# Optimization experiments

Measured on AMD Instinct MI355X. Metric: run time of the kernel, lower is better.

## Reference

```python
import jax, jax.numpy as jnp
import numpy as np

MARGIN = 1.0  # init kwarg
BIG = 1e9     # finite sentinel for masked reductions (dist in [0, 2])


def setup_inputs() -> dict:
    key = jax.random.key(0)
    k1, k2 = jax.random.split(key)
    embeddings = jax.random.normal(k1, (8192, 256), dtype=jnp.float32)
    labels = jax.random.randint(k2, (8192,), 0, 128)
    return {"embeddings": embeddings, "labels": labels}


def reference(embeddings, labels):
    # cosine distance matrix: 1 - x_hat @ x_hat^T, clamped at 0
    norm = jnp.linalg.norm(embeddings, axis=1, keepdims=True)
    x = embeddings / jnp.maximum(norm, 1e-12)  # matches F.normalize eps
    dist = jnp.clip(1.0 - x @ x.T, 0.0, None)  # (B, B)

    same = labels[:, None] == labels[None, :]
    eye = jnp.eye(labels.shape[0], dtype=bool)
    pos_mask = same & ~eye   # same label, different index
    neg_mask = ~same         # different label

    # hard mining: hardest positive (max dist), hardest negative (min dist)
    pos_dist = jnp.max(jnp.where(pos_mask, dist, -BIG), axis=1)  # (B,)
    neg_dist = jnp.min(jnp.where(neg_mask, dist, BIG), axis=1)   # (B,)

    valid = pos_mask.any(axis=1) & neg_mask.any(axis=1)          # (B,)
    per_anchor = jnp.maximum(pos_dist - neg_dist + MARGIN, 0.0)
    loss_sum = jnp.sum(jnp.where(valid, per_anchor, 0.0))
    count = jnp.sum(valid).astype(dist.dtype)
    return jnp.where(count > 0, loss_sum / jnp.maximum(count, 1.0), 0.0)
```

## Files before the change

kernel.cpp:

```cpp
#include <hip/hip_runtime.h>
#include <hip/hip_bf16.h>


constexpr int NB = 8192;
constexpr int ND = 256;
constexpr int BI = 256;
constexpr int BJ = 64;
constexpr int JSPLIT = 16;
constexpr int JRANGE = NB / JSPLIT;
constexpr int NITER = JRANGE / BJ;
constexpr int NCHUNK = ND / 8;

typedef __attribute__((ext_vector_type(8))) short bf16x8;
typedef __attribute__((ext_vector_type(4))) float f32x4;

typedef __attribute__((address_space(3))) unsigned int lds_u32;
typedef __attribute__((address_space(1))) const unsigned int g_u32;

__device__ inline void load_lds16(const unsigned short* g, unsigned short* l) {
    __builtin_amdgcn_global_load_lds((g_u32*)g, (lds_u32*)l, 16, 0, 0);
}

__device__ inline unsigned short f2bf(float v) {
    __hip_bfloat16 b = __float2bfloat16(v);
    return *reinterpret_cast<unsigned short*>(&b);
}

__global__ __launch_bounds__(256) void norm_kernel(const float* __restrict__ X,
                                                   unsigned short* __restrict__ Xbt,
                                                   float* accum, int* done) {
    __shared__ float tile[32][260];
    __shared__ float psum[32][8];
    __shared__ float rscale[32];
    const int t = threadIdx.x;
    const int rb = blockIdx.x * 32;
    if (blockIdx.x == 0 && t == 0) { accum[0] = 0.f; accum[1] = 0.f; *done = 0; }
    #pragma unroll
    for (int k = 0; k < 8; k++) {
        const int f = k * 256 + t;
        const int row = f >> 6, c4 = f & 63;
        const float4 v = *((const float4*)(X + (size_t)(rb + row) * ND) + c4);
        *(float4*)&tile[row][c4 * 4] = v;
    }
    __syncthreads();
    {
        const int r = t >> 3, e = t & 7;
        float s = 0.f;
        #pragma unroll
        for (int i = 0; i < 32; i++) { const float v = tile[r][e * 32 + i]; s += v * v; }
        psum[r][e] = s;
    }
    __syncthreads();
    if (t < 32) {
        float s = 0.f;
        #pragma unroll
        for (int e = 0; e < 8; e++) s += psum[t][e];
        rscale[t] = 1.0f / fmaxf(sqrtf(s), 1e-12f);
    }
    __syncthreads();
    #pragma unroll
    for (int j = 0; j < 4; j++) {
        const int idx = j * 256 + t;
        const int q = idx >> 5, r = idx & 31;
        const float sc = rscale[r];
        unsigned short tmp[8];
        #pragma unroll
        for (int e = 0; e < 8; e++) tmp[e] = f2bf(tile[r][q * 8 + e] * sc);
        *(bf16x8*)(Xbt + ((size_t)q * NB + rb + r) * 8) = *(bf16x8*)tmp;
    }
}

__global__ __launch_bounds__(256, 2) void mine_kernel(
    const unsigned short* __restrict__ Xbt, const int* __restrict__ labels,
    float* __restrict__ posP, float* __restrict__ negP) {
    __shared__ unsigned short Bt[32 * 512];
    __shared__ float Ljf[BJ];

    const int tid = threadIdx.x;
    const int w = tid >> 6;
    const int lane = tid & 63;
    const int quad = lane >> 4;
    const int l16 = lane & 15;

    const int rowbase = blockIdx.x * BI + w * 64;
    const int jstart = blockIdx.y * JRANGE;

    bf16x8 afrag[4][8];
    #pragma unroll
    for (int rs = 0; rs < 4; rs++)
        #pragma unroll
        for (int kc = 0; kc < 8; kc++) {
            const size_t u = (size_t)(kc * 4 + quad) * NB + (rowbase + rs * 16 + l16);
            afrag[rs][kc] = *(const bf16x8*)(Xbt + u * 8);
        }

    float flr[4][4];
    float minK[4][4], maxK[4][4];
    #pragma unroll
    for (int rs = 0; rs < 4; rs++)
        #pragma unroll
        for (int r = 0; r < 4; r++) {
            flr[rs][r] = (float)labels[rowbase + rs * 16 + quad * 4 + r];
            minK[rs][r] = 1e30f;
            maxK[rs][r] = -1e30f;
        }

    for (int jt = 0; jt < NITER; jt++) {
        const int jbase = jstart + jt * BJ;
        __syncthreads();
        #pragma unroll
        for (int s = 0; s < 8; s++) {
            const int rg = w * 8 + s;
            const int kc = rg >> 2, nfi = rg & 3;
            const size_t u = (size_t)(kc * 4 + quad) * NB + (jbase + nfi * 16 + l16);
            load_lds16(Xbt + u * 8, Bt + rg * 512);
        }
        if (tid < BJ) Ljf[tid] = (float)labels[jbase + tid];
        __syncthreads();

        #pragma unroll
        for (int nf = 0; nf < 4; nf++) {
            const float flc = Ljf[nf * 16 + l16];
            f32x4 acc[4];
            #pragma unroll
            for (int rs = 0; rs < 4; rs++) acc[rs] = (f32x4){0.f, 0.f, 0.f, 0.f};
            #pragma unroll
            for (int kc = 0; kc < 8; kc++) {
                const bf16x8 b = *(const bf16x8*)(Bt + (kc * 4 + nf) * 512 + lane * 8);
                #pragma unroll
                for (int rs = 0; rs < 4; rs++)
                    acc[rs] = __builtin_amdgcn_mfma_f32_16x16x32_bf16(
                        afrag[rs][kc], b, acc[rs], 0, 0, 0);
            }
            #pragma unroll
            for (int rs = 0; rs < 4; rs++)
                #pragma unroll
                for (int r = 0; r < 4; r++) {
                    const float d = flr[rs][r] - flc;
                    const float uu = fminf(fabsf(d), 1.0f);
                    const float key = fmaf(uu, 8.0f, acc[rs][r]);
                    minK[rs][r] = fminf(minK[rs][r], key);
                    maxK[rs][r] = fmaxf(maxK[rs][r], key);
                }
        }
    }

    #pragma unroll
    for (int rs = 0; rs < 4; rs++)
        #pragma unroll
        for (int r = 0; r < 4; r++) {
            float p = minK[rs][r], n = maxK[rs][r];
            #pragma unroll
            for (int m = 1; m <= 8; m <<= 1) {
                p = fminf(p, __shfl_xor(p, m, 64));
                n = fmaxf(n, __shfl_xor(n, m, 64));
            }
            if (l16 == 0) {
                const int row = rowbase + rs * 16 + quad * 4 + r;
                posP[blockIdx.y * NB + row] = p;
                negP[blockIdx.y * NB + row] = n;
            }
        }
}

__global__ __launch_bounds__(256) void finish_kernel(
    const float* __restrict__ posP, const float* __restrict__ negP,
    float* accum, int* done, float* __restrict__ out) {
    const int i = blockIdx.x * 256 + threadIdx.x;
    float p = 1e30f, n = -1e30f;
    #pragma unroll
    for (int s = 0; s < JSPLIT; s++) {
        p = fminf(p, posP[s * NB + i]);
        n = fmaxf(n, negP[s * NB + i]);
    }
    const bool valid = (p < 4.0f) && (n > 4.0f);
    const float pos_d = fmaxf(1.0f - p, 0.0f);
    const float neg_d = fmaxf(1.0f - (n - 8.0f), 0.0f);
    float per = valid ? fmaxf(pos_d - neg_d + 1.0f, 0.0f) : 0.0f;
    float cnt = valid ? 1.0f : 0.0f;
    #pragma unroll
    for (int off = 32; off > 0; off >>= 1) {
        per += __shfl_down(per, off, 64);
        cnt += __shfl_down(cnt, off, 64);
    }
    __shared__ float sp[4], sc[4];
    const int wv = threadIdx.x >> 6, ln = threadIdx.x & 63;
    if (ln == 0) { sp[wv] = per; sc[wv] = cnt; }
    __syncthreads();
    if (threadIdx.x == 0) {
        atomicAdd(&accum[0], sp[0] + sp[1] + sp[2] + sp[3]);
        atomicAdd(&accum[1], sc[0] + sc[1] + sc[2] + sc[3]);
        __threadfence();
        const int old = atomicAdd(done, 1);
        if (old == (int)gridDim.x - 1) {
            const float s = __hip_atomic_load(&accum[0], __ATOMIC_RELAXED,
                                              __HIP_MEMORY_SCOPE_AGENT);
            const float c = __hip_atomic_load(&accum[1], __ATOMIC_RELAXED,
                                              __HIP_MEMORY_SCOPE_AGENT);
            out[0] = (c > 0.f) ? s / fmaxf(c, 1.f) : 0.f;
        }
    }
}

extern "C" void kernel_launch(void* const* d_in, const int* in_sizes, int n_in,
                              void* d_out, int out_size, void* d_ws, size_t ws_size,
                              hipStream_t stream) {
    const float* X = (const float*)d_in[0];
    const int* labels = (const int*)d_in[1];
    float* out = (float*)d_out;

    char* ws = (char*)d_ws;
    unsigned short* Xbt = (unsigned short*)ws;
    float* posP = (float*)(ws + (size_t)4 * 1024 * 1024);
    float* negP = posP + JSPLIT * NB;
    float* accum = negP + JSPLIT * NB;
    int* done = (int*)(accum + 2);

    norm_kernel<<<NB / 32, 256, 0, stream>>>(X, Xbt, accum, done);
    mine_kernel<<<dim3(NB / BI, JSPLIT), 256, 0, stream>>>(
        (const unsigned short*)Xbt, labels, posP, negP);
    finish_kernel<<<NB / 256, 256, 0, stream>>>(posP, negP, accum, done, out);
}
```

Measured before the change: 98.97 us.

## Exploit distance symmetry with triangular tiles and atomic column/row reductions

Rewrites the mining kernel to compute only the upper-triangular 256x256 tiles of the symmetric similarity matrix. Each off-diagonal tile updates both row and column min/max keys through integer atomicMin/atomicMax on float bit patterns, offset by 2 so they stay positive. The separate finish kernel is folded into the last block to finish, using a ticket counter. This roughly halves the MFMA work and removes one launch and the partial-buffer traffic, at the cost of per-column shuffles and global atomics plus a serial tail done by one block.

```diff
diff --git a/kernel.cpp b/kernel.cpp
--- a/kernel.cpp
+++ b/kernel.cpp
@@ -4,12 +4,10 @@
 
 constexpr int NB = 8192;
 constexpr int ND = 256;
-constexpr int BI = 256;
+constexpr int TB = 256;
 constexpr int BJ = 64;
-constexpr int JSPLIT = 16;
-constexpr int JRANGE = NB / JSPLIT;
-constexpr int NITER = JRANGE / BJ;
-constexpr int NCHUNK = ND / 8;
+constexpr int NITER = TB / BJ;
+constexpr int NBLK = (NB / TB) * (NB / TB + 1) / 2;
 
 typedef __attribute__((ext_vector_type(8))) short bf16x8;
 typedef __attribute__((ext_vector_type(4))) float f32x4;
@@ -26,15 +24,20 @@
     return *reinterpret_cast<unsigned short*>(&b);
 }
 
+#define ENC6 0x40C00000u
+
 __global__ __launch_bounds__(256) void norm_kernel(const float* __restrict__ X,
                                                    unsigned short* __restrict__ Xbt,
-                                                   float* accum, int* done) {
+                                                   unsigned int* minKey,
+                                                   unsigned int* maxKey, int* done) {
     __shared__ float tile[32][260];
     __shared__ float psum[32][8];
     __shared__ float rscale[32];
     const int t = threadIdx.x;
     const int rb = blockIdx.x * 32;
-    if (blockIdx.x == 0 && t == 0) { accum[0] = 0.f; accum[1] = 0.f; *done = 0; }
+    const int g = blockIdx.x * 256 + t;
+    if (g < NB) { minKey[g] = 0xFFFFFFFFu; maxKey[g] = 0u; }
+    if (g == 0) *done = 0;
     #pragma unroll
     for (int k = 0; k < 8; k++) {
         const int f = k * 256 + t;
@@ -72,9 +75,20 @@
 
 __global__ __launch_bounds__(256, 2) void mine_kernel(
     const unsigned short* __restrict__ Xbt, const int* __restrict__ labels,
-    float* __restrict__ posP, float* __restrict__ negP) {
+    unsigned int* minKey, unsigned int* maxKey, int* done,
+    float* __restrict__ out) {
     __shared__ unsigned short Bt[32 * 512];
     __shared__ float Ljf[BJ];
+    __shared__ int ticket_s;
+
+    {   }
+    const int tb = blockIdx.x;
+    int a = (int)((sqrtf(8.0f * (float)tb + 1.0f) - 1.0f) * 0.5f);
+    while ((a + 1) * (a + 2) / 2 <= tb) a++;
+    while (a * (a + 1) / 2 > tb) a--;
+    const int Iblk = tb - a * (a + 1) / 2;
+    const int Jblk = a;
+    const bool isdiag = (Iblk == Jblk);
 
     const int tid = threadIdx.x;
     const int w = tid >> 6;
@@ -82,8 +96,7 @@
     const int quad = lane >> 4;
     const int l16 = lane & 15;
 
-    const int rowbase = blockIdx.x * BI + w * 64;
-    const int jstart = blockIdx.y * JRANGE;
+    const int rowbase = Iblk * TB + w * 64;
 
     bf16x8 afrag[4][8];
     #pragma unroll
@@ -94,8 +107,7 @@
             afrag[rs][kc] = *(const bf16x8*)(Xbt + u * 8);
         }
 
-    float flr[4][4];
-    float minK[4][4], maxK[4][4];
+    float flr[4][4], minK[4][4], maxK[4][4];
     #pragma unroll
     for (int rs = 0; rs < 4; rs++)
         #pragma unroll
@@ -106,7 +118,7 @@
         }
 
     for (int jt = 0; jt < NITER; jt++) {
-        const int jbase = jstart + jt * BJ;
+        const int jbase = Jblk * TB + jt * BJ;
         __syncthreads();
         #pragma unroll
         for (int s = 0; s < 8; s++) {
@@ -132,6 +144,7 @@
                     acc[rs] = __builtin_amdgcn_mfma_f32_16x16x32_bf16(
                         afrag[rs][kc], b, acc[rs], 0, 0, 0);
             }
+            float cMin = 1e30f, cMax = -1e30f;
             #pragma unroll
             for (int rs = 0; rs < 4; rs++)
                 #pragma unroll
@@ -141,7 +154,20 @@
                     const float key = fmaf(uu, 8.0f, acc[rs][r]);
                     minK[rs][r] = fminf(minK[rs][r], key);
                     maxK[rs][r] = fmaxf(maxK[rs][r], key);
+                    cMin = fminf(cMin, key);
+                    cMax = fmaxf(cMax, key);
                 }
+            if (!isdiag) {
+                cMin = fminf(cMin, __shfl_xor(cMin, 16, 64));
+                cMin = fminf(cMin, __shfl_xor(cMin, 32, 64));
+                cMax = fmaxf(cMax, __shfl_xor(cMax, 16, 64));
+                cMax = fmaxf(cMax, __shfl_xor(cMax, 32, 64));
+                if (quad == 0) {
+                    const int col = jbase + nf * 16 + l16;
+                    atomicMin(&minKey[col], __float_as_uint(cMin + 2.0f));
+                    atomicMax(&maxKey[col], __float_as_uint(cMax + 2.0f));
+                }
+            }
         }
     }
 
@@ -157,46 +183,42 @@
             }
             if (l16 == 0) {
                 const int row = rowbase + rs * 16 + quad * 4 + r;
-                posP[blockIdx.y * NB + row] = p;
-                negP[blockIdx.y * NB + row] = n;
-            }
-        }
-}
-
-__global__ __launch_bounds__(256) void finish_kernel(
-    const float* __restrict__ posP, const float* __restrict__ negP,
-    float* accum, int* done, float* __restrict__ out) {
-    const int i = blockIdx.x * 256 + threadIdx.x;
-    float p = 1e30f, n = -1e30f;
-    #pragma unroll
-    for (int s = 0; s < JSPLIT; s++) {
-        p = fminf(p, posP[s * NB + i]);
-        n = fmaxf(n, negP[s * NB + i]);
-    }
-    const bool valid = (p < 4.0f) && (n > 4.0f);
-    const float pos_d = fmaxf(1.0f - p, 0.0f);
-    const float neg_d = fmaxf(1.0f - (n - 8.0f), 0.0f);
-    float per = valid ? fmaxf(pos_d - neg_d + 1.0f, 0.0f) : 0.0f;
-    float cnt = valid ? 1.0f : 0.0f;
-    #pragma unroll
-    for (int off = 32; off > 0; off >>= 1) {
-        per += __shfl_down(per, off, 64);
-        cnt += __shfl_down(cnt, off, 64);
-    }
-    __shared__ float sp[4], sc[4];
-    const int wv = threadIdx.x >> 6, ln = threadIdx.x & 63;
-    if (ln == 0) { sp[wv] = per; sc[wv] = cnt; }
-    __syncthreads();
-    if (threadIdx.x == 0) {
-        atomicAdd(&accum[0], sp[0] + sp[1] + sp[2] + sp[3]);
-        atomicAdd(&accum[1], sc[0] + sc[1] + sc[2] + sc[3]);
+                atomicMin(&minKey[row], __float_as_uint(p + 2.0f));
+                atomicMax(&maxKey[row], __float_as_uint(n + 2.0f));
+            }
+        }
+
+    __threadfence();
+    __syncthreads();
+    if (tid == 0) ticket_s = atomicAdd(done, 1);
+    __syncthreads();
+    if (ticket_s == (int)gridDim.x - 1) {
         __threadfence();
-        const int old = atomicAdd(done, 1);
-        if (old == (int)gridDim.x - 1) {
-            const float s = __hip_atomic_load(&accum[0], __ATOMIC_RELAXED,
-                                              __HIP_MEMORY_SCOPE_AGENT);
-            const float c = __hip_atomic_load(&accum[1], __ATOMIC_RELAXED,
-                                              __HIP_MEMORY_SCOPE_AGENT);
+        float per = 0.f, cnt = 0.f;
+        #pragma unroll
+        for (int k = 0; k < NB / 256; k++) {
+            const int i = k * 256 + tid;
+            const unsigned int mk = minKey[i], xk = maxKey[i];
+            const bool valid = (mk < ENC6) && (xk > ENC6);
+            const float ps = __uint_as_float(mk) - 2.0f;
+            const float ns = __uint_as_float(xk) - 10.0f;
+            const float pd = fmaxf(1.0f - ps, 0.0f);
+            const float nd = fmaxf(1.0f - ns, 0.0f);
+            per += valid ? fmaxf(pd - nd + 1.0f, 0.0f) : 0.0f;
+            cnt += valid ? 1.0f : 0.0f;
+        }
+        #pragma unroll
+        for (int off = 32; off > 0; off >>= 1) {
+            per += __shfl_down(per, off, 64);
+            cnt += __shfl_down(cnt, off, 64);
+        }
+        __shared__ float sp[4], sc[4];
+        const int wv = tid >> 6, ln = tid & 63;
+        if (ln == 0) { sp[wv] = per; sc[wv] = cnt; }
+        __syncthreads();
+        if (tid == 0) {
+            const float s = sp[0] + sp[1] + sp[2] + sp[3];
+            const float c = sc[0] + sc[1] + sc[2] + sc[3];
             out[0] = (c > 0.f) ? s / fmaxf(c, 1.f) : 0.f;
         }
     }
@@ -211,13 +233,11 @@
 
     char* ws = (char*)d_ws;
     unsigned short* Xbt = (unsigned short*)ws;
-    float* posP = (float*)(ws + (size_t)4 * 1024 * 1024);
-    float* negP = posP + JSPLIT * NB;
-    float* accum = negP + JSPLIT * NB;
-    int* done = (int*)(accum + 2);
-
-    norm_kernel<<<NB / 32, 256, 0, stream>>>(X, Xbt, accum, done);
-    mine_kernel<<<dim3(NB / BI, JSPLIT), 256, 0, stream>>>(
-        (const unsigned short*)Xbt, labels, posP, negP);
-    finish_kernel<<<NB / 256, 256, 0, stream>>>(posP, negP, accum, done, out);
-}
+    unsigned int* minKey = (unsigned int*)(ws + (size_t)4 * 1024 * 1024);
+    unsigned int* maxKey = minKey + NB;
+    int* done = (int*)(maxKey + NB);
+
+    norm_kernel<<<NB / 32, 256, 0, stream>>>(X, Xbt, minKey, maxKey, done);
+    mine_kernel<<<NBLK, 256, 0, stream>>>(
+        (const unsigned short*)Xbt, labels, minKey, maxKey, done, out);
+}
```

Result: slower. 147.9 us (+49.4%).
